# Kernel tuning notes

Hardware: AMD Instinct MI355X
Metric: run time of the kernel (lower is better)

The kernel has to match this reference:

```python
import jax, jax.numpy as jnp
import numpy as np

K = 4        # Legendre orders / channels
T = 1024     # sequence length (== max_len)
B = 2        # batch
D = 256      # feature dim
THETA = 200.0  # LegT window length; dt = 1/theta


def _make_hippo_legt(N):
    # A_{nk} = -sqrt((2n+1)(2k+1)) * sigma_{nk}; B_n = sqrt(2n+1)
    n = np.arange(N, dtype=np.float64)
    P = np.sqrt(2.0 * n + 1.0)
    PP = P[:, None] * P[None, :]
    diff = n[:, None] - n[None, :]
    sign = np.ones_like(PP)
    upper = diff < 0
    sign[upper] = (-1.0) ** (-diff[upper])
    A = -PP * sign
    Bv = P.reshape(N, 1)
    return A, Bv


def _legt_kernel(T_, N, theta):
    """M[k] = Abar^k @ Bbar, k = 0..T-1 (bilinear discretization, dt=1/theta)."""
    A, Bv = _make_hippo_legt(N)
    dt = 1.0 / float(theta)
    I = np.eye(N)
    inv = np.linalg.inv(I - 0.5 * dt * A)
    Abar = inv @ (I + 0.5 * dt * A)
    Bbar = (inv @ (Bv * dt)).squeeze(-1)
    M = np.zeros((T_, N), dtype=np.float64)
    cur = Bbar.copy()
    for k in range(T_):
        M[k] = cur
        cur = Abar @ cur
    return M.astype(np.float32)


def setup_inputs() -> dict:
    key = jax.random.key(0)
    h = jax.random.normal(key, (B, T, D), dtype=jnp.float32)
    M = jnp.asarray(_legt_kernel(T, K, THETA))  # (T, K) precomputed buffer
    return {"h": h, "M": M}


def reference(h, M):
    # c[b, t, k, d] = sum_{s<=t} M[t-s, k] * h[b, s, d]
    B_, T_, d = h.shape
    t = jnp.arange(T_)
    ix = t[:, None] - t[None, :]                    # (T, T)
    mask = (ix >= 0).astype(h.dtype)
    W = M[jnp.clip(ix, 0)] * mask[:, :, None]       # (T, T, K) causal Toeplitz bank
    return jnp.einsum('tsk,bsd->btkd', W, h)        # (B, T, K, D)
```

## Files before the change

kernel.cpp:

```cpp
#include <hip/hip_runtime.h>
#include <math.h>

namespace {

constexpr int K_ = 4;
constexpr int T_ = 1024;
constexpr int B_ = 2;
constexpr int D_ = 256;

constexpr int CHUNKS = 16;
constexpr int L_ = T_ / CHUNKS;
constexpr int G_ = 16;
constexpr int BLOCK = G_ * CHUNKS;
constexpr int GRID = (B_ * D_) / G_;

__device__ __forceinline__ void compute_consts(float Af[4][4], float Bf[4],
                                               float ALf[4][4]) {
    const double dt = 1.0 / 200.0;
    double P[4], A[4][4];
#pragma unroll
    for (int n = 0; n < 4; ++n) P[n] = sqrt(2.0 * n + 1.0);
#pragma unroll
    for (int n = 0; n < 4; ++n)
#pragma unroll
        for (int k = 0; k < 4; ++k) {
            double s = (n >= k) ? 1.0 : (((k - n) & 1) ? -1.0 : 1.0);
            A[n][k] = -P[n] * P[k] * s;
        }
    double aug[4][9];
#pragma unroll
    for (int r = 0; r < 4; ++r) {
#pragma unroll
        for (int c = 0; c < 4; ++c) {
            double idc = (r == c) ? 1.0 : 0.0;
            aug[r][c]     = idc - 0.5 * dt * A[r][c];
            aug[r][4 + c] = idc + 0.5 * dt * A[r][c];
        }
        aug[r][8] = P[r] * dt;
    }
#pragma unroll
    for (int p = 0; p < 4; ++p) {
        double pinv = 1.0 / aug[p][p];
#pragma unroll
        for (int c = 0; c < 9; ++c) aug[p][c] *= pinv;
#pragma unroll
        for (int r = 0; r < 4; ++r) {
            if (r == p) continue;
            double f = aug[r][p];
#pragma unroll
            for (int c = 0; c < 9; ++c) aug[r][c] -= f * aug[p][c];
        }
    }
#pragma unroll
    for (int r = 0; r < 4; ++r) {
#pragma unroll
        for (int c = 0; c < 4; ++c) Af[r][c] = (float)aug[r][4 + c];
        Bf[r] = (float)aug[r][8];
    }
    float X[4][4];
#pragma unroll
    for (int r = 0; r < 4; ++r)
#pragma unroll
        for (int c = 0; c < 4; ++c) X[r][c] = Af[r][c];
#pragma unroll
    for (int s = 0; s < 6; ++s) {
        float Y[4][4];
#pragma unroll
        for (int r = 0; r < 4; ++r)
#pragma unroll
            for (int c = 0; c < 4; ++c) {
                float acc = 0.f;
#pragma unroll
                for (int k = 0; k < 4; ++k) acc = fmaf(X[r][k], X[k][c], acc);
                Y[r][c] = acc;
            }
#pragma unroll
        for (int r = 0; r < 4; ++r)
#pragma unroll
            for (int c = 0; c < 4; ++c) X[r][c] = Y[r][c];
    }
#pragma unroll
    for (int r = 0; r < 4; ++r)
#pragma unroll
        for (int c = 0; c < 4; ++c) ALf[r][c] = X[r][c];
}

__global__ __launch_bounds__(BLOCK) void hippo_scan(
    const float* __restrict__ h, const float* __restrict__ M,
    float* __restrict__ out)
{
    const int tid   = threadIdx.x;
    const int lane  = tid & (G_ - 1);
    const int chunk = tid >> 4;
    const int g = blockIdx.x * G_ + lane;
    const int b = g >> 8;
    const int d = g & (D_ - 1);

    const float* hp = h + (size_t)(b * T_ + chunk * L_) * D_ + d;

    float y0 = 0.f, y1 = 0.f, y2 = 0.f, y3 = 0.f;
#pragma unroll 8
    for (int i = 0; i < L_; ++i) {
        float hv = hp[i * D_];
        const float* mr = M + (L_ - 1 - i) * K_;
        y0 = fmaf(mr[0], hv, y0);
        y1 = fmaf(mr[1], hv, y1);
        y2 = fmaf(mr[2], hv, y2);
        y3 = fmaf(mr[3], hv, y3);
    }

    __shared__ float yst[CHUNKS][G_][K_];
    __shared__ float ini[CHUNKS][G_][K_];
    yst[chunk][lane][0] = y0; yst[chunk][lane][1] = y1;
    yst[chunk][lane][2] = y2; yst[chunk][lane][3] = y3;

    float Af[4][4], Bf[4], ALf[4][4];
    compute_consts(Af, Bf, ALf);

    __syncthreads();

    if (tid < G_) {
        float x0 = 0.f, x1 = 0.f, x2 = 0.f, x3 = 0.f;
#pragma unroll
        for (int c = 0; c < CHUNKS; ++c) {
            ini[c][tid][0] = x0; ini[c][tid][1] = x1;
            ini[c][tid][2] = x2; ini[c][tid][3] = x3;
            float e0 = yst[c][tid][0], e1 = yst[c][tid][1];
            float e2 = yst[c][tid][2], e3 = yst[c][tid][3];
            float n0 = fmaf(ALf[0][0], x0, fmaf(ALf[0][1], x1, fmaf(ALf[0][2], x2, fmaf(ALf[0][3], x3, e0))));
            float n1 = fmaf(ALf[1][0], x0, fmaf(ALf[1][1], x1, fmaf(ALf[1][2], x2, fmaf(ALf[1][3], x3, e1))));
            float n2 = fmaf(ALf[2][0], x0, fmaf(ALf[2][1], x1, fmaf(ALf[2][2], x2, fmaf(ALf[2][3], x3, e2))));
            float n3 = fmaf(ALf[3][0], x0, fmaf(ALf[3][1], x1, fmaf(ALf[3][2], x2, fmaf(ALf[3][3], x3, e3))));
            x0 = n0; x1 = n1; x2 = n2; x3 = n3;
        }
    }
    __syncthreads();

    float x0 = ini[chunk][lane][0], x1 = ini[chunk][lane][1];
    float x2 = ini[chunk][lane][2], x3 = ini[chunk][lane][3];

    float* op = out + (size_t)(b * T_ + chunk * L_) * K_ * D_ + d;
#pragma unroll 4
    for (int i = 0; i < L_; ++i) {
        float hv = hp[i * D_];
        float n0 = fmaf(Af[0][0], x0, fmaf(Af[0][1], x1, fmaf(Af[0][2], x2, fmaf(Af[0][3], x3, Bf[0] * hv))));
        float n1 = fmaf(Af[1][0], x0, fmaf(Af[1][1], x1, fmaf(Af[1][2], x2, fmaf(Af[1][3], x3, Bf[1] * hv))));
        float n2 = fmaf(Af[2][0], x0, fmaf(Af[2][1], x1, fmaf(Af[2][2], x2, fmaf(Af[2][3], x3, Bf[2] * hv))));
        float n3 = fmaf(Af[3][0], x0, fmaf(Af[3][1], x1, fmaf(Af[3][2], x2, fmaf(Af[3][3], x3, Bf[3] * hv))));
        x0 = n0; x1 = n1; x2 = n2; x3 = n3;
        op[0 * D_] = x0; op[1 * D_] = x1; op[2 * D_] = x2; op[3 * D_] = x3;
        op += K_ * D_;
    }
}

}

extern "C" void kernel_launch(void* const* d_in, const int* in_sizes, int n_in,
                              void* d_out, int out_size, void* d_ws, size_t ws_size,
                              hipStream_t stream) {
    const float* h = (const float*)d_in[0];
    const float* M = (const float*)d_in[1];
    float* out = (float*)d_out;
    hippo_scan<<<GRID, BLOCK, 0, stream>>>(h, M, out);
}
```

Before: 65.61 us.

## Split chunked scan into three kernels with parallel Hillis-Steele cross-chunk scan

Replaces the single fused kernel (16 chunks of 64 steps, 32 blocks) with three launches. The first computes per-chunk partial states for 128 chunks of 8 steps. The second runs a log-depth Hillis-Steele scan over those chunks using precomputed powers of the transition matrix. The third re-runs the recurrence and writes the outputs. This removes the long serial chunk loop and the low block count of the old kernel. In exchange it adds two extra launches, a round trip through workspace memory, and a second full read of h.

```diff
diff --git a/kernel.cpp b/kernel.cpp
--- a/kernel.cpp
+++ b/kernel.cpp
@@ -7,15 +7,13 @@
 constexpr int T_ = 1024;
 constexpr int B_ = 2;
 constexpr int D_ = 256;
+constexpr int NSEQ = B_ * D_;
 
-constexpr int CHUNKS = 16;
-constexpr int L_ = T_ / CHUNKS;
-constexpr int G_ = 16;
-constexpr int BLOCK = G_ * CHUNKS;
-constexpr int GRID = (B_ * D_) / G_;
+constexpr int CH = 128;
+constexpr int L_ = T_ / CH;
+constexpr int LOG_CH = 7;
 
-__device__ __forceinline__ void compute_consts(float Af[4][4], float Bf[4],
-                                               float ALf[4][4]) {
+__device__ __forceinline__ void base_consts(float Af[4][4], float Bf[4]) {
     const double dt = 1.0 / 200.0;
     double P[4], A[4][4];
 #pragma unroll
@@ -57,49 +55,56 @@
         for (int c = 0; c < 4; ++c) Af[r][c] = (float)aug[r][4 + c];
         Bf[r] = (float)aug[r][8];
     }
-    float X[4][4];
+}
+
+__device__ __forceinline__ void matsq(const float X[4][4], float Y[4][4]) {
 #pragma unroll
     for (int r = 0; r < 4; ++r)
 #pragma unroll
-        for (int c = 0; c < 4; ++c) X[r][c] = Af[r][c];
+        for (int c = 0; c < 4; ++c) {
+            float acc = 0.f;
 #pragma unroll
-    for (int s = 0; s < 6; ++s) {
-        float Y[4][4];
+            for (int k = 0; k < 4; ++k) acc = fmaf(X[r][k], X[k][c], acc);
+            Y[r][c] = acc;
+        }
+}
+
+__device__ __forceinline__ void scan_consts(float AP[LOG_CH][4][4]) {
+    float Af[4][4], Bf[4];
+    base_consts(Af, Bf);
+    float X[4][4], Y[4][4];
+    matsq(Af, X);
+    matsq(X, Y);
+    matsq(Y, X);
+#pragma unroll
+    for (int s = 0; s < LOG_CH; ++s) {
 #pragma unroll
         for (int r = 0; r < 4; ++r)
 #pragma unroll
-            for (int c = 0; c < 4; ++c) {
-                float acc = 0.f;
-#pragma unroll
-                for (int k = 0; k < 4; ++k) acc = fmaf(X[r][k], X[k][c], acc);
-                Y[r][c] = acc;
-            }
+            for (int c = 0; c < 4; ++c) AP[s][r][c] = X[r][c];
+        matsq(X, Y);
 #pragma unroll
         for (int r = 0; r < 4; ++r)
 #pragma unroll
             for (int c = 0; c < 4; ++c) X[r][c] = Y[r][c];
     }
-#pragma unroll
-    for (int r = 0; r < 4; ++r)
-#pragma unroll
-        for (int c = 0; c < 4; ++c) ALf[r][c] = X[r][c];
 }
 
-__global__ __launch_bounds__(BLOCK) void hippo_scan(
+__global__ __launch_bounds__(256) void k1a_chunk_states(
     const float* __restrict__ h, const float* __restrict__ M,
-    float* __restrict__ out)
+    float* __restrict__ ws_y)
 {
-    const int tid   = threadIdx.x;
-    const int lane  = tid & (G_ - 1);
-    const int chunk = tid >> 4;
-    const int g = blockIdx.x * G_ + lane;
-    const int b = g >> 8;
-    const int d = g & (D_ - 1);
+    const int dlane = threadIdx.x & 63;
+    const int csub  = threadIdx.x >> 6;
+    const int sg    = blockIdx.x & 7;
+    const int cg    = blockIdx.x >> 3;
+    const int seq = sg * 64 + dlane;
+    const int b = seq >> 8, d = seq & (D_ - 1);
+    const int c = cg * 4 + csub;
 
-    const float* hp = h + (size_t)(b * T_ + chunk * L_) * D_ + d;
-
+    const float* hp = h + ((size_t)(b * T_ + c * L_)) * D_ + d;
     float y0 = 0.f, y1 = 0.f, y2 = 0.f, y3 = 0.f;
-#pragma unroll 8
+#pragma unroll
     for (int i = 0; i < L_; ++i) {
         float hv = hp[i * D_];
         const float* mr = M + (L_ - 1 - i) * K_;
@@ -108,39 +113,59 @@
         y2 = fmaf(mr[2], hv, y2);
         y3 = fmaf(mr[3], hv, y3);
     }
+    float4* wp = (float4*)ws_y + (size_t)c * NSEQ + seq;
+    *wp = make_float4(y0, y1, y2, y3);
+}
 
-    __shared__ float yst[CHUNKS][G_][K_];
-    __shared__ float ini[CHUNKS][G_][K_];
-    yst[chunk][lane][0] = y0; yst[chunk][lane][1] = y1;
-    yst[chunk][lane][2] = y2; yst[chunk][lane][3] = y3;
+__global__ __launch_bounds__(256) void k1b_scan(
+    const float* __restrict__ ws_y, float* __restrict__ ws_init)
+{
+    const int sp = threadIdx.x & 1;
+    const int c  = threadIdx.x >> 1;
+    const int seq = blockIdx.x * 2 + sp;
 
-    float Af[4][4], Bf[4], ALf[4][4];
-    compute_consts(Af, Bf, ALf);
+    float AP[LOG_CH][4][4];
+    scan_consts(AP);
 
-    __syncthreads();
+    float4 v = ((const float4*)ws_y)[(size_t)c * NSEQ + seq];
 
-    if (tid < G_) {
-        float x0 = 0.f, x1 = 0.f, x2 = 0.f, x3 = 0.f;
+    __shared__ float4 lds[CH * 2];
 #pragma unroll
-        for (int c = 0; c < CHUNKS; ++c) {
-            ini[c][tid][0] = x0; ini[c][tid][1] = x1;
-            ini[c][tid][2] = x2; ini[c][tid][3] = x3;
-            float e0 = yst[c][tid][0], e1 = yst[c][tid][1];
-            float e2 = yst[c][tid][2], e3 = yst[c][tid][3];
-            float n0 = fmaf(ALf[0][0], x0, fmaf(ALf[0][1], x1, fmaf(ALf[0][2], x2, fmaf(ALf[0][3], x3, e0))));
-            float n1 = fmaf(ALf[1][0], x0, fmaf(ALf[1][1], x1, fmaf(ALf[1][2], x2, fmaf(ALf[1][3], x3, e1))));
-            float n2 = fmaf(ALf[2][0], x0, fmaf(ALf[2][1], x1, fmaf(ALf[2][2], x2, fmaf(ALf[2][3], x3, e2))));
-            float n3 = fmaf(ALf[3][0], x0, fmaf(ALf[3][1], x1, fmaf(ALf[3][2], x2, fmaf(ALf[3][3], x3, e3))));
-            x0 = n0; x1 = n1; x2 = n2; x3 = n3;
+    for (int s = 0; s < LOG_CH; ++s) {
+        const int off = 1 << s;
+        lds[threadIdx.x] = v;
+        __syncthreads();
+        if (c >= off) {
+            float4 p = lds[threadIdx.x - off * 2];
+            v.x = fmaf(AP[s][0][0], p.x, fmaf(AP[s][0][1], p.y, fmaf(AP[s][0][2], p.z, fmaf(AP[s][0][3], p.w, v.x))));
+            v.y = fmaf(AP[s][1][0], p.x, fmaf(AP[s][1][1], p.y, fmaf(AP[s][1][2], p.z, fmaf(AP[s][1][3], p.w, v.y))));
+            v.z = fmaf(AP[s][2][0], p.x, fmaf(AP[s][2][1], p.y, fmaf(AP[s][2][2], p.z, fmaf(AP[s][2][3], p.w, v.z))));
+            v.w = fmaf(AP[s][3][0], p.x, fmaf(AP[s][3][1], p.y, fmaf(AP[s][3][2], p.z, fmaf(AP[s][3][3], p.w, v.w))));
         }
+        __syncthreads();
     }
-    __syncthreads();
+    float4* ip = (float4*)ws_init;
+    if (c < CH - 1) ip[(size_t)(c + 1) * NSEQ + seq] = v;
+    if (c == 0)     ip[seq] = make_float4(0.f, 0.f, 0.f, 0.f);
+}
 
-    float x0 = ini[chunk][lane][0], x1 = ini[chunk][lane][1];
-    float x2 = ini[chunk][lane][2], x3 = ini[chunk][lane][3];
+__global__ __launch_bounds__(256) void k2_emit(
+    const float* __restrict__ h, const float* __restrict__ ws_init,
+    float* __restrict__ out)
+{
+    const int d = threadIdx.x;
+    const int c = blockIdx.x & (CH - 1);
+    const int b = blockIdx.x >> LOG_CH;
 
-    float* op = out + (size_t)(b * T_ + chunk * L_) * K_ * D_ + d;
-#pragma unroll 4
+    float Af[4][4], Bf[4];
+    base_consts(Af, Bf);
+
+    float4 xi = ((const float4*)ws_init)[(size_t)c * NSEQ + b * D_ + d];
+    float x0 = xi.x, x1 = xi.y, x2 = xi.z, x3 = xi.w;
+
+    const float* hp = h + ((size_t)(b * T_ + c * L_)) * D_ + d;
+    float* op = out + ((size_t)(b * T_ + c * L_)) * K_ * D_ + d;
+#pragma unroll
     for (int i = 0; i < L_; ++i) {
         float hv = hp[i * D_];
         float n0 = fmaf(Af[0][0], x0, fmaf(Af[0][1], x1, fmaf(Af[0][2], x2, fmaf(Af[0][3], x3, Bf[0] * hv))));
@@ -161,5 +186,11 @@
     const float* h = (const float*)d_in[0];
     const float* M = (const float*)d_in[1];
     float* out = (float*)d_out;
-    hippo_scan<<<GRID, BLOCK, 0, stream>>>(h, M, out);
+
+    float* ws_y    = (float*)d_ws;
+    float* ws_init = ws_y + (size_t)CH * NSEQ * K_;
+
+    k1a_chunk_states<<<(NSEQ / 64) * (CH / 4), 256, 0, stream>>>(h, M, ws_y);
+    k1b_scan<<<NSEQ / 2, 256, 0, stream>>>(ws_y, ws_init);
+    k2_emit<<<B_ * CH, 256, 0, stream>>>(h, ws_init, out);
 }
```

After: 63.68 us. -2.9%, faster.
